# Kernel optimization log

Hardware: AMD Instinct MI355X
Metric: run time of the kernel (lower is better)

## Reference

```python
import jax, jax.numpy as jnp
import numpy as np

N_NODES = 100000
N_EDGES = 1600000
HIDDEN = 64
LEAKY_SLOPE = 0.01  # torch F.leaky_relu default


def setup_inputs() -> dict:
    key = jax.random.key(0)
    k1, k2, k3, k4 = jax.random.split(key, 4)
    x = jax.random.normal(k1, (N_NODES, HIDDEN), dtype=jnp.float32)
    edge_index = jax.random.randint(k2, (2, N_EDGES), 0, N_NODES, dtype=jnp.int64)
    # Linear(hidden, 1, bias=False) weights, squeezed to [hidden]
    w_i = jax.random.normal(k3, (HIDDEN,), dtype=jnp.float32) * 0.1
    w_j = jax.random.normal(k4, (HIDDEN,), dtype=jnp.float32) * 0.1
    return {"x": x, "edge_index": edge_index, "w_i": w_i, "w_j": w_j}


def reference(x, edge_index, w_i, w_j):
    n = x.shape[0]
    ej, ei = edge_index[0], edge_index[1]  # (edge_index_j, edge_index_i)
    # per-node attention scores, then per-edge gather
    s_i = x @ w_i  # [N]
    s_j = x @ w_j  # [N]
    e = jax.nn.leaky_relu(s_i[ei] + s_j[ej], LEAKY_SLOPE)  # [E]
    # segment softmax over edges grouped by destination node ei
    emax = jax.ops.segment_max(e, ei, num_segments=n)  # [N]
    ex = jnp.exp(e - emax[ei])  # [E]
    denom = jax.ops.segment_sum(ex, ei, num_segments=n)  # [N]
    alpha = ex / denom[ei]  # [E]
    # spmm: out[i] = sum_{edges e: dst=i} alpha_e * x[src_e]
    out = jax.ops.segment_sum(alpha[:, None] * x[ej], ei, num_segments=n)  # [N, H]
    return jax.nn.relu(out)
```

## Files before the change

### kernel.cpp

```cpp
#include <hip/hip_runtime.h>
#include <stdint.h>

#define N_NODES 100000
#define N_EDGES 1600000
#define HIDDEN  64
#define SLOPE   0.01f
#define NBUCK   782
#define CAPB    2816
#define PCHUNK  16384
#define NPART   98
#define NSB     391
#define NCAP    48
#define NSTRIDE 50


__device__ __forceinline__ unsigned short f2bf(float f) {
    uint32_t u = __float_as_uint(f);
    uint32_t r = u + 0x7FFFu + ((u >> 16) & 1u);
    return (unsigned short)(r >> 16);
}

__device__ __forceinline__ float bflo(uint32_t d) { return __uint_as_float(d << 16); }
__device__ __forceinline__ float bfhi(uint32_t d) { return __uint_as_float(d & 0xFFFF0000u); }

__global__ void __launch_bounds__(1024) k_build(const float* __restrict__ x,
                                                const float* __restrict__ w_i,
                                                const float* __restrict__ w_j,
                                                const int* __restrict__ srcs,
                                                const int* __restrict__ dsts,
                                                float* __restrict__ s_i,
                                                float* __restrict__ s_j,
                                                unsigned short* __restrict__ xb,
                                                int* __restrict__ ctrl,
                                                uint32_t* __restrict__ pairs) {
    __shared__ int lcnt[NBUCK], lloc[NBUCK], lbase[NBUCK];
    __shared__ int wsum[16];
    __shared__ uint32_t srec[PCHUNK];
    int tid = threadIdx.x;
    if (blockIdx.x < NPART) {
        if (tid < NBUCK) lcnt[tid] = 0;
        __syncthreads();
        int e0 = blockIdx.x * PCHUNK;
        int e1 = min(e0 + PCHUNK, N_EDGES);
        for (int e = e0 + tid; e < e1; e += 1024)
            atomicAdd(&lcnt[dsts[e] >> 7], 1);
        __syncthreads();
        int v = (tid < NBUCK) ? lcnt[tid] : 0;
        int pre = v;
#pragma unroll
        for (int off = 1; off < 64; off <<= 1) {
            int t = __shfl_up(pre, off, 64);
            if ((tid & 63) >= off) pre += t;
        }
        if ((tid & 63) == 63) wsum[tid >> 6] = pre;
        __syncthreads();
        if (tid < 16) {
            int s = wsum[tid];
#pragma unroll
            for (int off = 1; off < 16; off <<= 1) {
                int t = __shfl_up(s, off, 64);
                if (tid >= off) s += t;
            }
            wsum[tid] = s;
        }
        __syncthreads();
        int wavebase = (tid >> 6) ? wsum[(tid >> 6) - 1] : 0;
        if (tid < NBUCK) {
            lloc[tid] = wavebase + pre - v;
            lbase[tid] = v ? atomicAdd(&ctrl[tid], v) : 0;
            lcnt[tid] = 0;
        }
        __syncthreads();
        for (int e = e0 + tid; e < e1; e += 1024) {
            int src = srcs[e];
            int dst = dsts[e];
            int b = dst >> 7;
            int r = atomicAdd(&lcnt[b], 1);
            srec[lloc[b] + r] = ((uint32_t)(dst & 127) << 24) | (uint32_t)src;
        }
        __syncthreads();
        int wv = tid >> 6, ln = tid & 63;
        for (int b = wv; b < NBUCK; b += 16) {
            int c = lcnt[b];
            int lo = lloc[b], go = lbase[b];
            for (int j = ln; j < c; j += 64) {
                int pos = go + j;
                if (pos < CAPB)
                    pairs[(size_t)b * CAPB + pos] = srec[lo + j];
            }
        }
        return;
    }
    int u0 = blockIdx.x - NPART;
    int g16 = tid >> 4;
    int ql = tid & 15;
    float4 wi4 = ((const float4*)w_i)[ql];
    float4 wj4 = ((const float4*)w_j)[ql];
#pragma unroll
    for (int i = 0; i < 4; ++i) {
        int node = u0 * 256 + i * 64 + g16;
        if (node >= N_NODES) break;
        float4 v = ((const float4*)x)[node * 16 + ql];
        float a = v.x * wi4.x + v.y * wi4.y + v.z * wi4.z + v.w * wi4.w;
        float b = v.x * wj4.x + v.y * wj4.y + v.z * wj4.z + v.w * wj4.w;
#pragma unroll
        for (int off = 1; off < 16; off <<= 1) {
            a += __shfl_xor(a, off, 64);
            b += __shfl_xor(b, off, 64);
        }
        if (ql == 0) { s_i[node] = a; s_j[node] = b; }
        ushort4 o;
        o.x = f2bf(v.x); o.y = f2bf(v.y); o.z = f2bf(v.z); o.w = f2bf(v.w);
        ((ushort4*)xb)[node * 16 + ql] = o;
    }
}

__global__ void __launch_bounds__(1024, 8) k_bucket_agg(const uint2* __restrict__ xw2,
                                                        const uint32_t* __restrict__ pairs,
                                                        const int* __restrict__ ctrl,
                                                        const float* __restrict__ s_i,
                                                        const float* __restrict__ s_j,
                                                        float* __restrict__ out) {
    __shared__ uint64_t spairs[128 * NSTRIDE];
    __shared__ int lcur[128];
    __shared__ float s_si[128];
    int tid = threadIdx.x;
    int cb = blockIdx.x;
    int node0 = cb * 128;
    const uint32_t* reg = pairs + (size_t)cb * CAPB;
    int rcnt = min(ctrl[cb], CAPB);
    for (int i = tid; i < 128 * NSTRIDE; i += 1024) spairs[i] = 0ull;
    if (tid < 128) {
        lcur[tid] = 0;
        int node = node0 + tid;
        s_si[tid] = (node < N_NODES) ? s_i[node] : 0.f;
    }
    __syncthreads();
    {
        int e0 = tid, e1 = tid + 1024;
        bool a0 = e0 < rcnt, a1 = e1 < rcnt;
        uint32_t p0 = a0 ? reg[e0] : 0u;
        uint32_t p1 = a1 ? reg[e1] : 0u;
        float sj0 = a0 ? s_j[p0 & 0xFFFFFFu] : 0.f;
        float sj1 = a1 ? s_j[p1 & 0xFFFFFFu] : 0.f;
        if (a0) {
            int n = (int)(p0 >> 24);
            float sc = s_si[n] + sj0;
            sc = (sc > 0.f) ? sc : SLOPE * sc;
            float w = __expf(sc);
            int slot = atomicAdd(&lcur[n], 1);
            if (slot < NCAP)
                spairs[n * NSTRIDE + slot] =
                    ((uint64_t)__float_as_uint(w) << 32) | (p0 & 0xFFFFFFu);
        }
        if (a1) {
            int n = (int)(p1 >> 24);
            float sc = s_si[n] + sj1;
            sc = (sc > 0.f) ? sc : SLOPE * sc;
            float w = __expf(sc);
            int slot = atomicAdd(&lcur[n], 1);
            if (slot < NCAP)
                spairs[n * NSTRIDE + slot] =
                    ((uint64_t)__float_as_uint(w) << 32) | (p1 & 0xFFFFFFu);
        }
        for (int e = tid + 2048; e < rcnt; e += 1024) {
            uint32_t p = reg[e];
            int n = (int)(p >> 24);
            float sc = s_si[n] + s_j[p & 0xFFFFFFu];
            sc = (sc > 0.f) ? sc : SLOPE * sc;
            float w = __expf(sc);
            int slot = atomicAdd(&lcur[n], 1);
            if (slot < NCAP)
                spairs[n * NSTRIDE + slot] =
                    ((uint64_t)__float_as_uint(w) << 32) | (p & 0xFFFFFFu);
        }
    }
    __syncthreads();
    int wave = tid >> 6, lane = tid & 63;
    int quarter = (lane >> 4) & 3;
    int l16 = lane & 15;
    int kA = wave * 8 + quarter;
    int kB = kA + 4;
    int nodeA = node0 + kA, nodeB = node0 + kB;
    int cA = lcur[kA], cB = lcur[kB];
    int cqA = min(cA, NCAP), cqB = min(cB, NCAP);
    int mx = max(cqA, cqB);
    mx = max(mx, __shfl_xor(mx, 16, 64));
    mx = max(mx, __shfl_xor(mx, 32, 64));
    const uint64_t* ppA = spairs + kA * NSTRIDE;
    const uint64_t* ppB = spairs + kB * NSTRIDE;
    float accA[4] = {0.f, 0.f, 0.f, 0.f};
    float accB[4] = {0.f, 0.f, 0.f, 0.f};
    float denA = 0.f, denB = 0.f;
    for (int j = 0; j < mx; j += 4) {
        uint64_t rA[4], rB[4];
#pragma unroll
        for (int t = 0; t < 4; ++t) { rA[t] = ppA[j + t]; rB[t] = ppB[j + t]; }
        uint2 dA[4], dB[4];
#pragma unroll
        for (int t = 0; t < 4; ++t)
            dA[t] = xw2[((uint32_t)rA[t] & 0xFFFFFFu) * 16 + l16];
#pragma unroll
        for (int t = 0; t < 4; ++t)
            dB[t] = xw2[((uint32_t)rB[t] & 0xFFFFFFu) * 16 + l16];
        __builtin_amdgcn_sched_barrier(0);
#pragma unroll
        for (int t = 0; t < 4; ++t) {
            float w = __uint_as_float((uint32_t)(rA[t] >> 32));
            denA += w;
            accA[0] = fmaf(w, bflo(dA[t].x), accA[0]);
            accA[1] = fmaf(w, bfhi(dA[t].x), accA[1]);
            accA[2] = fmaf(w, bflo(dA[t].y), accA[2]);
            accA[3] = fmaf(w, bfhi(dA[t].y), accA[3]);
        }
#pragma unroll
        for (int t = 0; t < 4; ++t) {
            float w = __uint_as_float((uint32_t)(rB[t] >> 32));
            denB += w;
            accB[0] = fmaf(w, bflo(dB[t].x), accB[0]);
            accB[1] = fmaf(w, bfhi(dB[t].x), accB[1]);
            accB[2] = fmaf(w, bflo(dB[t].y), accB[2]);
            accB[3] = fmaf(w, bfhi(dB[t].y), accB[3]);
        }
    }
    if (cA > NCAP) {
        denA = 0.f;
#pragma unroll
        for (int i = 0; i < 4; ++i) accA[i] = 0.f;
        for (int e = 0; e < rcnt; ++e) {
            uint32_t p = reg[e];
            if ((int)(p >> 24) == kA) {
                uint32_t src = p & 0xFFFFFFu;
                float sc = s_si[kA] + s_j[src];
                sc = (sc > 0.f) ? sc : SLOPE * sc;
                float w = __expf(sc);
                uint2 d = xw2[src * 16 + l16];
                denA += w;
                accA[0] = fmaf(w, bflo(d.x), accA[0]);
                accA[1] = fmaf(w, bfhi(d.x), accA[1]);
                accA[2] = fmaf(w, bflo(d.y), accA[2]);
                accA[3] = fmaf(w, bfhi(d.y), accA[3]);
            }
        }
    }
    if (cB > NCAP) {
        denB = 0.f;
#pragma unroll
        for (int i = 0; i < 4; ++i) accB[i] = 0.f;
        for (int e = 0; e < rcnt; ++e) {
            uint32_t p = reg[e];
            if ((int)(p >> 24) == kB) {
                uint32_t src = p & 0xFFFFFFu;
                float sc = s_si[kB] + s_j[src];
                sc = (sc > 0.f) ? sc : SLOPE * sc;
                float w = __expf(sc);
                uint2 d = xw2[src * 16 + l16];
                denB += w;
                accB[0] = fmaf(w, bflo(d.x), accB[0]);
                accB[1] = fmaf(w, bfhi(d.x), accB[1]);
                accB[2] = fmaf(w, bflo(d.y), accB[2]);
                accB[3] = fmaf(w, bfhi(d.y), accB[3]);
            }
        }
    }
    if (nodeA < N_NODES) {
        float4 r = make_float4(0.f, 0.f, 0.f, 0.f);
        if (cA > 0) {
            float inv = 1.f / denA;
            r.x = fmaxf(accA[0] * inv, 0.f);
            r.y = fmaxf(accA[1] * inv, 0.f);
            r.z = fmaxf(accA[2] * inv, 0.f);
            r.w = fmaxf(accA[3] * inv, 0.f);
        }
        ((float4*)(out + (size_t)nodeA * HIDDEN))[l16] = r;
    }
    if (nodeB < N_NODES) {
        float4 r = make_float4(0.f, 0.f, 0.f, 0.f);
        if (cB > 0) {
            float inv = 1.f / denB;
            r.x = fmaxf(accB[0] * inv, 0.f);
            r.y = fmaxf(accB[1] * inv, 0.f);
            r.z = fmaxf(accB[2] * inv, 0.f);
            r.w = fmaxf(accB[3] * inv, 0.f);
        }
        ((float4*)(out + (size_t)nodeB * HIDDEN))[l16] = r;
    }
}

extern "C" void kernel_launch(void* const* d_in, const int* in_sizes, int n_in,
                              void* d_out, int out_size, void* d_ws, size_t ws_size,
                              hipStream_t stream) {
    const float* x   = (const float*)d_in[0];
    const int*   ei  = (const int*)d_in[1];
    const float* w_i = (const float*)d_in[2];
    const float* w_j = (const float*)d_in[3];
    float* out = (float*)d_out;

    char* p = (char*)d_ws;
    float*          s_i   = (float*)p;          p += (size_t)N_NODES * 4;
    float*          s_j   = (float*)p;          p += (size_t)N_NODES * 4;
    unsigned short* xb    = (unsigned short*)p; p += (size_t)N_NODES * HIDDEN * 2;
    int*            ctrl  = (int*)p;            p += 4096;
    uint32_t*       pairs = (uint32_t*)p;

    const int* srcs = ei;
    const int* dsts = ei + N_EDGES;

    hipMemsetAsync(ctrl, 0, (NBUCK + 1) * sizeof(int), stream);
    k_build     <<<NPART + NSB, 1024, 0, stream>>>(x, w_i, w_j, srcs, dsts,
                                                   s_i, s_j, xb, ctrl, pairs);
    k_bucket_agg<<<NBUCK, 1024, 0, stream>>>((const uint2*)xb, pairs, ctrl,
                                             s_i, s_j, out);
}
```

Before: 150.2 us.

## Sub-bin bucket edge records by source range to localize gathers

Each destination bucket's edge list is split into four sub-bins keyed by source node range, using wave ballots and per-bin atomic offsets during the scatter. The aggregation kernel then walks the bins in order, so consecutive edges gather s_j and bf16 x rows from a narrower source range, which is meant to improve cache locality. The cost is more ballot and popcount work and more global atomics in the build phase, and a fixed per-bin capacity that could overflow where the old per-bucket cap would not have.

Result: slower. 178.5 us (+18.8%).

```diff
diff --git a/kernel.cpp b/kernel.cpp
--- a/kernel.cpp
+++ b/kernel.cpp
@@ -6,7 +6,9 @@
 #define HIDDEN  64
 #define SLOPE   0.01f
 #define NBUCK   782
-#define CAPB    2816
+#define NBIN    4
+#define BINW    25000
+#define CAPBIN  768
 #define PCHUNK  16384
 #define NPART   98
 #define NSB     391
@@ -33,7 +35,7 @@
                                                 unsigned short* __restrict__ xb,
                                                 int* __restrict__ ctrl,
                                                 uint32_t* __restrict__ pairs) {
-    __shared__ int lcnt[NBUCK], lloc[NBUCK], lbase[NBUCK];
+    __shared__ int lcnt[NBUCK], lloc[NBUCK];
     __shared__ int wsum[16];
     __shared__ uint32_t srec[PCHUNK];
     int tid = threadIdx.x;
@@ -67,7 +69,6 @@
         int wavebase = (tid >> 6) ? wsum[(tid >> 6) - 1] : 0;
         if (tid < NBUCK) {
             lloc[tid] = wavebase + pre - v;
-            lbase[tid] = v ? atomicAdd(&ctrl[tid], v) : 0;
             lcnt[tid] = 0;
         }
         __syncthreads();
@@ -82,11 +83,37 @@
         int wv = tid >> 6, ln = tid & 63;
         for (int b = wv; b < NBUCK; b += 16) {
             int c = lcnt[b];
-            int lo = lloc[b], go = lbase[b];
-            for (int j = ln; j < c; j += 64) {
-                int pos = go + j;
-                if (pos < CAPB)
-                    pairs[(size_t)b * CAPB + pos] = srec[lo + j];
+            int lo = lloc[b];
+            for (int j0 = 0; j0 < c; j0 += 64) {
+                int j = j0 + ln;
+                bool valid = j < c;
+                uint32_t r = valid ? srec[lo + j] : 0u;
+                int bin = valid ? (int)((r & 0xFFFFFFu) / BINW) : NBIN;
+                unsigned long long m0 = __ballot(bin == 0);
+                unsigned long long m1 = __ballot(bin == 1);
+                unsigned long long m2 = __ballot(bin == 2);
+                unsigned long long m3 = __ballot(bin == 3);
+                int myBase = 0;
+                if (ln < NBIN) {
+                    unsigned long long mm = (ln == 0) ? m0 : (ln == 1) ? m1
+                                          : (ln == 2) ? m2 : m3;
+                    int cnt = __popcll(mm);
+                    if (cnt) myBase = atomicAdd(&ctrl[b * NBIN + ln], cnt);
+                }
+                int b0 = __shfl(myBase, 0, 64);
+                int b1 = __shfl(myBase, 1, 64);
+                int b2 = __shfl(myBase, 2, 64);
+                int b3 = __shfl(myBase, 3, 64);
+                if (valid) {
+                    unsigned long long mm = (bin == 0) ? m0 : (bin == 1) ? m1
+                                          : (bin == 2) ? m2 : m3;
+                    int rank = __popcll(mm & ((1ull << ln) - 1ull));
+                    int base = (bin == 0) ? b0 : (bin == 1) ? b1
+                             : (bin == 2) ? b2 : b3;
+                    int pos = base + rank;
+                    if (pos < CAPBIN)
+                        pairs[((size_t)b * NBIN + bin) * CAPBIN + pos] = r;
+                }
             }
         }
         return;
@@ -127,8 +154,12 @@
     int tid = threadIdx.x;
     int cb = blockIdx.x;
     int node0 = cb * 128;
-    const uint32_t* reg = pairs + (size_t)cb * CAPB;
-    int rcnt = min(ctrl[cb], CAPB);
+    const uint32_t* rg = pairs + (size_t)cb * NBIN * CAPBIN;
+    int rc0 = min(ctrl[cb * NBIN + 0], CAPBIN);
+    int rc1 = min(ctrl[cb * NBIN + 1], CAPBIN);
+    int rc2 = min(ctrl[cb * NBIN + 2], CAPBIN);
+    int rc3 = min(ctrl[cb * NBIN + 3], CAPBIN);
+    int p1 = rc0, p2 = rc0 + rc1, p3 = rc0 + rc1 + rc2, tot = p3 + rc3;
     for (int i = tid; i < 128 * NSTRIDE; i += 1024) spairs[i] = 0ull;
     if (tid < 128) {
         lcur[tid] = 0;
@@ -136,44 +167,18 @@
         s_si[tid] = (node < N_NODES) ? s_i[node] : 0.f;
     }
     __syncthreads();
-    {
-        int e0 = tid, e1 = tid + 1024;
-        bool a0 = e0 < rcnt, a1 = e1 < rcnt;
-        uint32_t p0 = a0 ? reg[e0] : 0u;
-        uint32_t p1 = a1 ? reg[e1] : 0u;
-        float sj0 = a0 ? s_j[p0 & 0xFFFFFFu] : 0.f;
-        float sj1 = a1 ? s_j[p1 & 0xFFFFFFu] : 0.f;
-        if (a0) {
-            int n = (int)(p0 >> 24);
-            float sc = s_si[n] + sj0;
-            sc = (sc > 0.f) ? sc : SLOPE * sc;
-            float w = __expf(sc);
-            int slot = atomicAdd(&lcur[n], 1);
-            if (slot < NCAP)
-                spairs[n * NSTRIDE + slot] =
-                    ((uint64_t)__float_as_uint(w) << 32) | (p0 & 0xFFFFFFu);
-        }
-        if (a1) {
-            int n = (int)(p1 >> 24);
-            float sc = s_si[n] + sj1;
-            sc = (sc > 0.f) ? sc : SLOPE * sc;
-            float w = __expf(sc);
-            int slot = atomicAdd(&lcur[n], 1);
-            if (slot < NCAP)
-                spairs[n * NSTRIDE + slot] =
-                    ((uint64_t)__float_as_uint(w) << 32) | (p1 & 0xFFFFFFu);
-        }
-        for (int e = tid + 2048; e < rcnt; e += 1024) {
-            uint32_t p = reg[e];
-            int n = (int)(p >> 24);
-            float sc = s_si[n] + s_j[p & 0xFFFFFFu];
-            sc = (sc > 0.f) ? sc : SLOPE * sc;
-            float w = __expf(sc);
-            int slot = atomicAdd(&lcur[n], 1);
-            if (slot < NCAP)
-                spairs[n * NSTRIDE + slot] =
-                    ((uint64_t)__float_as_uint(w) << 32) | (p & 0xFFFFFFu);
-        }
+    for (int e = tid; e < tot; e += 1024) {
+        int w = (e >= p1) + (e >= p2) + (e >= p3);
+        int idx = e - ((w == 0) ? 0 : (w == 1) ? p1 : (w == 2) ? p2 : p3);
+        uint32_t p = rg[(size_t)w * CAPBIN + idx];
+        int n = (int)(p >> 24);
+        float sc = s_si[n] + s_j[p & 0xFFFFFFu];
+        sc = (sc > 0.f) ? sc : SLOPE * sc;
+        float wgt = __expf(sc);
+        int slot = atomicAdd(&lcur[n], 1);
+        if (slot < NCAP)
+            spairs[n * NSTRIDE + slot] =
+                ((uint64_t)__float_as_uint(wgt) << 32) | (p & 0xFFFFFFu);
     }
     __syncthreads();
     int wave = tid >> 6, lane = tid & 63;
@@ -227,19 +232,22 @@
         denA = 0.f;
 #pragma unroll
         for (int i = 0; i < 4; ++i) accA[i] = 0.f;
-        for (int e = 0; e < rcnt; ++e) {
-            uint32_t p = reg[e];
-            if ((int)(p >> 24) == kA) {
-                uint32_t src = p & 0xFFFFFFu;
-                float sc = s_si[kA] + s_j[src];
-                sc = (sc > 0.f) ? sc : SLOPE * sc;
-                float w = __expf(sc);
-                uint2 d = xw2[src * 16 + l16];
-                denA += w;
-                accA[0] = fmaf(w, bflo(d.x), accA[0]);
-                accA[1] = fmaf(w, bfhi(d.x), accA[1]);
-                accA[2] = fmaf(w, bflo(d.y), accA[2]);
-                accA[3] = fmaf(w, bfhi(d.y), accA[3]);
+        for (int w4 = 0; w4 < NBIN; ++w4) {
+            int rc = min(ctrl[cb * NBIN + w4], CAPBIN);
+            for (int e = 0; e < rc; ++e) {
+                uint32_t p = rg[(size_t)w4 * CAPBIN + e];
+                if ((int)(p >> 24) == kA) {
+                    uint32_t src = p & 0xFFFFFFu;
+                    float sc = s_si[kA] + s_j[src];
+                    sc = (sc > 0.f) ? sc : SLOPE * sc;
+                    float w = __expf(sc);
+                    uint2 d = xw2[src * 16 + l16];
+                    denA += w;
+                    accA[0] = fmaf(w, bflo(d.x), accA[0]);
+                    accA[1] = fmaf(w, bfhi(d.x), accA[1]);
+                    accA[2] = fmaf(w, bflo(d.y), accA[2]);
+                    accA[3] = fmaf(w, bfhi(d.y), accA[3]);
+                }
             }
         }
     }
@@ -247,19 +255,22 @@
         denB = 0.f;
 #pragma unroll
         for (int i = 0; i < 4; ++i) accB[i] = 0.f;
-        for (int e = 0; e < rcnt; ++e) {
-            uint32_t p = reg[e];
-            if ((int)(p >> 24) == kB) {
-                uint32_t src = p & 0xFFFFFFu;
-                float sc = s_si[kB] + s_j[src];
-                sc = (sc > 0.f) ? sc : SLOPE * sc;
-                float w = __expf(sc);
-                uint2 d = xw2[src * 16 + l16];
-                denB += w;
-                accB[0] = fmaf(w, bflo(d.x), accB[0]);
-                accB[1] = fmaf(w, bfhi(d.x), accB[1]);
-                accB[2] = fmaf(w, bflo(d.y), accB[2]);
-                accB[3] = fmaf(w, bfhi(d.y), accB[3]);
+        for (int w4 = 0; w4 < NBIN; ++w4) {
+            int rc = min(ctrl[cb * NBIN + w4], CAPBIN);
+            for (int e = 0; e < rc; ++e) {
+                uint32_t p = rg[(size_t)w4 * CAPBIN + e];
+                if ((int)(p >> 24) == kB) {
+                    uint32_t src = p & 0xFFFFFFu;
+                    float sc = s_si[kB] + s_j[src];
+                    sc = (sc > 0.f) ? sc : SLOPE * sc;
+                    float w = __expf(sc);
+                    uint2 d = xw2[src * 16 + l16];
+                    denB += w;
+                    accB[0] = fmaf(w, bflo(d.x), accB[0]);
+                    accB[1] = fmaf(w, bfhi(d.x), accB[1]);
+                    accB[2] = fmaf(w, bflo(d.y), accB[2]);
+                    accB[3] = fmaf(w, bfhi(d.y), accB[3]);
+                }
             }
         }
     }
@@ -300,13 +311,13 @@
     float*          s_i   = (float*)p;          p += (size_t)N_NODES * 4;
     float*          s_j   = (float*)p;          p += (size_t)N_NODES * 4;
     unsigned short* xb    = (unsigned short*)p; p += (size_t)N_NODES * HIDDEN * 2;
-    int*            ctrl  = (int*)p;            p += 4096;
+    int*            ctrl  = (int*)p;            p += 16384;
     uint32_t*       pairs = (uint32_t*)p;
 
     const int* srcs = ei;
     const int* dsts = ei + N_EDGES;
 
-    hipMemsetAsync(ctrl, 0, (NBUCK + 1) * sizeof(int), stream);
+    hipMemsetAsync(ctrl, 0, NBUCK * NBIN * sizeof(int), stream);
     k_build     <<<NPART + NSB, 1024, 0, stream>>>(x, w_i, w_j, srcs, dsts,
                                                    s_i, s_j, xb, ctrl, pairs);
     k_bucket_agg<<<NBUCK, 1024, 0, stream>>>((const uint2*)xb, pairs, ctrl,
```
